# Performance work log

Measured on AMD Instinct MI355X. Metric: run time of the kernel, lower is better.

Reference implementation:

```python
import jax, jax.numpy as jnp
import numpy as np

N, F_IN, C, H, E, G = 10000, 128, 256, 4, 160000, 512
BN_EPS = 1e-5


def setup_inputs() -> dict:
    key = jax.random.key(0)
    ks = iter(jax.random.split(key, 40))
    nrm = lambda shape, s=0.05: jax.random.normal(next(ks), shape, jnp.float32) * s

    def bn(dim):
        # rows: gamma, beta, running_mean, running_var (eval-mode BatchNorm)
        g = 1.0 + jax.random.normal(next(ks), (dim,), jnp.float32) * 0.1
        b = jax.random.normal(next(ks), (dim,), jnp.float32) * 0.1
        m = jax.random.normal(next(ks), (dim,), jnp.float32) * 0.1
        v = jax.random.uniform(next(ks), (dim,), jnp.float32, 0.5, 1.5)
        return jnp.stack([g, b, m, v])  # [4, dim]

    x = jax.random.normal(next(ks), (N, F_IN), jnp.float32)
    edge_index = jax.random.randint(next(ks), (2, E), 0, N, jnp.int64)
    batch = (jnp.arange(N, dtype=jnp.int64) * G) // N  # sorted, every graph non-empty

    return {
        "x": x, "edge_index": edge_index, "batch": batch,
        "W1": nrm((F_IN, H * C)), "att_src1": nrm((H, C)), "att_dst1": nrm((H, C)), "b1": nrm((H * C,)), "bn1": bn(H * C),
        "W2": nrm((H * C, H * C)), "att_src2": nrm((H, C)), "att_dst2": nrm((H, C)), "b2": nrm((H * C,)), "bn2": bn(H * C),
        "W3": nrm((H * C, C)), "att_src3": nrm((1, C)), "att_dst3": nrm((1, C)), "b3": nrm((C,)), "bn3": bn(C),
        "fc1_w": nrm((3 * C, 2 * C)), "fc1_b": nrm((2 * C,)), "bnf1": bn(2 * C),
        "fc2_w": nrm((2 * C, C)), "fc2_b": nrm((C,)), "bnf2": bn(C),
        "fc3_w": nrm((C, 1)), "fc3_b": nrm((1,)),
    }


def batchnorm(x, p):
    g, b, m, v = p
    return (x - m) * (g * jax.lax.rsqrt(v + BN_EPS)) + b


def gat_conv(x, src, dst, W, att_src, att_dst, bias, heads):
    n = x.shape[0]
    h = (x @ W).reshape(n, heads, -1)                      # [N,H,C]
    a_src = jnp.einsum('nhc,hc->nh', h, att_src)           # [N,H]
    a_dst = jnp.einsum('nhc,hc->nh', h, att_dst)
    logits = jax.nn.leaky_relu(a_src[src] + a_dst[dst], 0.2)  # [E,H]
    # scatter-softmax over incoming edges of each destination node
    m = jax.ops.segment_max(logits, dst, num_segments=n)
    m = jax.lax.stop_gradient(jnp.where(jnp.isfinite(m), m, 0.0))
    e = jnp.exp(logits - m[dst])
    denom = jax.ops.segment_sum(e, dst, num_segments=n)
    alpha = e / (denom[dst] + 1e-16)                       # [E,H]
    msg = h[src] * alpha[:, :, None]                       # [E,H,C]
    out = jax.ops.segment_sum(msg, dst, num_segments=n)    # [N,H,C]
    return out.reshape(n, -1) + bias


def reference(x, edge_index, batch,
              W1, att_src1, att_dst1, b1, bn1,
              W2, att_src2, att_dst2, b2, bn2,
              W3, att_src3, att_dst3, b3, bn3,
              fc1_w, fc1_b, bnf1, fc2_w, fc2_b, bnf2, fc3_w, fc3_b):
    src, dst = edge_index[0], edge_index[1]
    h = jax.nn.elu(batchnorm(gat_conv(x, src, dst, W1, att_src1, att_dst1, b1, H), bn1))
    h = jax.nn.elu(batchnorm(gat_conv(h, src, dst, W2, att_src2, att_dst2, b2, H), bn2))
    h = jax.nn.elu(batchnorm(gat_conv(h, src, dst, W3, att_src3, att_dst3, b3, 1), bn3))
    # multi-pool readout over graphs
    s = jax.ops.segment_sum(h, batch, num_segments=G)
    cnt = jax.ops.segment_sum(jnp.ones((h.shape[0], 1), h.dtype), batch, num_segments=G)
    mean = s / cnt
    mx = jax.ops.segment_max(h, batch, num_segments=G)
    z = jnp.concatenate([mean, mx, s], axis=1)             # [G, 3C]
    z = jax.nn.relu(batchnorm(z @ fc1_w + fc1_b, bnf1))    # dropout: eval mode (identity)
    z = jax.nn.relu(batchnorm(z @ fc2_w + fc2_b, bnf2))
    return z @ fc3_w + fc3_b                               # [G, 1]
```

## Files before the change

### kernel.cpp

```cpp
#include <hip/hip_runtime.h>
#include <math.h>

#define N_NODES 10000
#define N_EDGES 160000
#define N_GRAPH 512

#define NEG_INF (-1e30f)

typedef __attribute__((ext_vector_type(8))) short s16x8;
typedef __attribute__((ext_vector_type(4))) float f32x4;

__device__ __forceinline__ unsigned short f2b(float f) {
  union { float f; unsigned u; } c{f};
  unsigned u = c.u;
  return (unsigned short)((u + 0x7fff + ((u >> 16) & 1)) >> 16);
}
__device__ __forceinline__ float b2f(unsigned short h) {
  union { unsigned u; float f; } c{(unsigned)h << 16};
  return c.f;
}

#define GLL16(gp, lp)                                                          \
  __builtin_amdgcn_global_load_lds(                                            \
      (const __attribute__((address_space(1))) unsigned int*)(gp),             \
      (__attribute__((address_space(3))) unsigned int*)(lp), 16, 0, 0)

__global__ void k_count(const int* __restrict__ dst, const int* __restrict__ batch,
                        int* __restrict__ deg, int* __restrict__ gcnt) {
  int i = blockIdx.x * 256 + threadIdx.x;
  if (i < N_EDGES) atomicAdd(&deg[dst[i]], 1);
  if (i < N_NODES) atomicAdd(&gcnt[batch[i]], 1);
}

__global__ void k_scan(const int* __restrict__ in, int* __restrict__ out, int n) {
  __shared__ int buf[1024];
  __shared__ int carry_s;
  if (threadIdx.x == 0) carry_s = 0;
  __syncthreads();
  for (int base = 0; base < n; base += 1024) {
    int i = base + (int)threadIdx.x;
    int v = (i < n) ? in[i] : 0;
    buf[threadIdx.x] = v;
    __syncthreads();
    for (int off = 1; off < 1024; off <<= 1) {
      int t = (threadIdx.x >= (unsigned)off) ? buf[threadIdx.x - off] : 0;
      __syncthreads();
      buf[threadIdx.x] += t;
      __syncthreads();
    }
    int carry = carry_s;
    if (i < n) out[i] = carry + buf[threadIdx.x] - v;
    __syncthreads();
    if (threadIdx.x == 0) carry_s = carry + buf[1023];
    __syncthreads();
  }
  if (threadIdx.x == 0) out[n] = carry_s;
}

__global__ void k_fill(const int* __restrict__ src, const int* __restrict__ dst,
                       const int* __restrict__ rowoff, int* __restrict__ cursor,
                       int* __restrict__ csr) {
  int e = blockIdx.x * 256 + threadIdx.x;
  if (e < N_EDGES) {
    int d = dst[e];
    int p = atomicAdd(&cursor[d], 1);
    csr[rowoff[d] + p] = src[e];
  }
}

__global__ __launch_bounds__(256) void k_sortseg(const int* __restrict__ rowoff,
                                                 int* __restrict__ vals) {
  const int node = blockIdx.x * 4 + (threadIdx.x >> 6);
  if (node >= N_NODES) return;
  const int lane = threadIdx.x & 63;
  const int a = rowoff[node], b = rowoff[node + 1];
  const int deg = b - a;
  if (deg <= 1) return;
  if (deg <= 64) {
    int v = (lane < deg) ? vals[a + lane] : 0x7fffffff;
#pragma unroll
    for (int ph = 0; ph < 64; ++ph) {
      const int par = ph & 1;
      const bool left = ((lane & 1) == par);
      const int partner = left ? lane + 1 : lane - 1;
      const int pv = __shfl(v, partner & 63);
      if (partner >= 0 && partner < 64) v = left ? min(v, pv) : max(v, pv);
    }
    if (lane < deg) vals[a + lane] = v;
  } else if (lane == 0) {
    for (int p = a + 1; p < b; ++p) {
      int v = vals[p];
      int q = p - 1;
      while (q >= a && vals[q] > v) { vals[q + 1] = vals[q]; --q; }
      vals[q + 1] = v;
    }
  }
}

__global__ void k_f2b4(const float* __restrict__ in, unsigned short* __restrict__ out, int n4) {
  int i = blockIdx.x * 256 + threadIdx.x;
  if (i < n4) {
    float4 v = ((const float4*)in)[i];
    ushort4 o;
    o.x = f2b(v.x); o.y = f2b(v.y); o.z = f2b(v.z); o.w = f2b(v.w);
    ((ushort4*)out)[i] = o;
  }
}

__global__ __launch_bounds__(256) void k_convT(const float* __restrict__ in,
                                               unsigned short* __restrict__ out,
                                               int K, int M) {
  __shared__ float t[32][33];
  const int mb = blockIdx.x * 32, kb = blockIdx.y * 32;
  const int tx = threadIdx.x & 31, ty = threadIdx.x >> 5;
#pragma unroll
  for (int r = ty; r < 32; r += 8) t[r][tx] = in[(size_t)(kb + r) * M + mb + tx];
  __syncthreads();
#pragma unroll
  for (int r = ty; r < 32; r += 8)
    out[(size_t)(mb + r) * K + kb + tx] = f2b(t[tx][r]);
}

__global__ __launch_bounds__(256) void k_gemm_bf16(
    const unsigned short* __restrict__ A, const unsigned short* __restrict__ Bt,
    unsigned short* __restrict__ Cbf, int M, int N, int K) {
  __shared__ unsigned short As[128 * 32];
  __shared__ unsigned short Bs[128 * 32];
  const int tid = threadIdx.x;
  const int lane = tid & 63, wave = tid >> 6;
  const int wr = wave >> 1, wc = wave & 1;
  const int m0 = blockIdx.y * 128, n0 = blockIdx.x * 128;

  f32x4 acc[4][4];
#pragma unroll
  for (int i = 0; i < 4; ++i)
#pragma unroll
    for (int j = 0; j < 4; ++j) acc[i][j] = (f32x4){0.f, 0.f, 0.f, 0.f};

  const int l4 = lane >> 2;
  const int kp8 = (lane & 3) * 8;
  int rA0 = m0 + wave * 32 + l4;
  int rA1 = rA0 + 16;
  rA0 = min(rA0, M - 1);
  rA1 = min(rA1, M - 1);
  const int rB0 = n0 + wave * 32 + l4;
  const int rB1 = rB0 + 16;
  const unsigned short* pA0 = A + (size_t)rA0 * K + kp8;
  const unsigned short* pA1 = A + (size_t)rA1 * K + kp8;
  const unsigned short* pB0 = Bt + (size_t)rB0 * K + kp8;
  const unsigned short* pB1 = Bt + (size_t)rB1 * K + kp8;
  unsigned short* lA = As + wave * 1024;
  unsigned short* lB = Bs + wave * 1024;

  const int fr = lane & 15, kg = (lane >> 4) * 8;

  for (int kb = 0; kb < K; kb += 32) {
    GLL16(pA0 + kb, lA);
    GLL16(pA1 + kb, lA + 512);
    GLL16(pB0 + kb, lB);
    GLL16(pB1 + kb, lB + 512);
    __syncthreads();

    s16x8 a[4], b[4];
#pragma unroll
    for (int m = 0; m < 4; ++m)
      a[m] = *(const s16x8*)&As[(wr * 64 + m * 16 + fr) * 32 + kg];
#pragma unroll
    for (int n = 0; n < 4; ++n)
      b[n] = *(const s16x8*)&Bs[(wc * 64 + n * 16 + fr) * 32 + kg];
#pragma unroll
    for (int m = 0; m < 4; ++m)
#pragma unroll
      for (int n = 0; n < 4; ++n)
        acc[m][n] = __builtin_amdgcn_mfma_f32_16x16x32_bf16(a[m], b[n], acc[m][n], 0, 0, 0);
    __syncthreads();
  }

  const int frow = (lane >> 4) * 4;
#pragma unroll
  for (int m = 0; m < 4; ++m) {
#pragma unroll
    for (int r = 0; r < 4; ++r) {
      const int row = m0 + wr * 64 + m * 16 + frow + r;
      if (row < M) {
#pragma unroll
        for (int n = 0; n < 4; ++n) {
          const int col = n0 + wc * 64 + n * 16 + fr;
          Cbf[(size_t)row * N + col] = f2b(acc[m][n][r]);
        }
      }
    }
  }
}

template <int K, int M>
__global__ __launch_bounds__(256) void k_head_fc(
    const float* __restrict__ A, const float* __restrict__ W,
    float* __restrict__ C, const float* __restrict__ bias,
    const float* __restrict__ bn) {
  constexpr int KQ = K / 4;
  __shared__ float Ap[8 * K];
  __shared__ float part[4][8][64];
  const int tid = threadIdx.x;
  const int g0 = blockIdx.y * 8;
  const int m0 = blockIdx.x * 64;
  const int c = tid & 63;
  const int q = tid >> 6;

  for (int i = tid; i < 8 * K / 4; i += 256)
    ((float4*)Ap)[i] = ((const float4*)(A + (size_t)g0 * K))[i];
  __syncthreads();

  float acc[8];
#pragma unroll
  for (int r = 0; r < 8; ++r) acc[r] = 0.f;

  const float* Wc = W + m0 + c;
  const int k0 = q * KQ;
  for (int k = k0; k < k0 + KQ; k += 4) {
    float wv[4];
#pragma unroll
    for (int u = 0; u < 4; ++u) wv[u] = Wc[(size_t)(k + u) * M];
#pragma unroll
    for (int r = 0; r < 8; ++r) {
      const float4 a4 = *(const float4*)&Ap[r * K + k];
      acc[r] += a4.x * wv[0] + a4.y * wv[1] + a4.z * wv[2] + a4.w * wv[3];
    }
  }

#pragma unroll
  for (int r = 0; r < 8; ++r) part[q][r][c] = acc[r];
  __syncthreads();

  for (int i = tid; i < 512; i += 256) {
    const int r = i >> 6, cc = i & 63;
    float v = part[0][r][cc] + part[1][r][cc] + part[2][r][cc] + part[3][r][cc];
    const int gc = m0 + cc;
    v += bias[gc];
    const float g = bn[gc], b = bn[M + gc], mu = bn[2 * M + gc], var = bn[3 * M + gc];
    v = (v - mu) * (g * rsqrtf(var + 1e-5f)) + b;
    v = fmaxf(v, 0.f);
    C[(size_t)(g0 + r) * M + gc] = v;
  }
}

template <int HEADS>
__global__ __launch_bounds__(64) void k_att(const unsigned short* __restrict__ h,
                                            const float* __restrict__ att_s,
                                            const float* __restrict__ att_d,
                                            float* __restrict__ aS,
                                            float* __restrict__ aD) {
  const int b = blockIdx.x;
  const int node = b / HEADS, hd = b % HEADS;
  const int lane = threadIdx.x;
  const unsigned short* row = h + (size_t)node * HEADS * 256 + hd * 256;
  const ushort4 v = *(const ushort4*)&row[lane * 4];
  const float4 s4 = *(const float4*)&att_s[hd * 256 + lane * 4];
  const float4 d4 = *(const float4*)&att_d[hd * 256 + lane * 4];
  float ss = b2f(v.x) * s4.x + b2f(v.y) * s4.y + b2f(v.z) * s4.z + b2f(v.w) * s4.w;
  float sd = b2f(v.x) * d4.x + b2f(v.y) * d4.y + b2f(v.z) * d4.z + b2f(v.w) * d4.w;
#pragma unroll
  for (int off = 32; off; off >>= 1) {
    ss += __shfl_xor(ss, off);
    sd += __shfl_xor(sd, off);
  }
  if (lane == 0) {
    aS[node * HEADS + hd] = ss;
    aD[node * HEADS + hd] = sd;
  }
}

template <int HEADS, int OUTBF>
__global__ __launch_bounds__(256) void k_gat_agg(
    const unsigned short* __restrict__ hpre, const float* __restrict__ aS,
    const float* __restrict__ aD, const int* __restrict__ rowoff,
    const int* __restrict__ csr, const float* __restrict__ bias,
    const float* __restrict__ bn, unsigned short* __restrict__ outb,
    float* __restrict__ outf) {
  constexpr int HC = HEADS * 256;
  constexpr int CPT = HC / 256;
  const int node = blockIdx.x;
  const int tid = threadIdx.x;
  const int lane = tid & 63, wave = tid >> 6;
  const int r0 = rowoff[node], r1 = rowoff[node + 1];
  const int deg = r1 - r0;

  __shared__ float s_m[HEADS], s_d[HEADS];
  __shared__ float s_alpha[HEADS * 64];
  __shared__ int s_src[64];

  if (wave < HEADS) {
    const float adn = aD[node * HEADS + wave];
    float mx = NEG_INF;
    for (int i = lane; i < deg; i += 64) {
      int s = csr[r0 + i];
      float l = aS[s * HEADS + wave] + adn;
      l = l > 0.f ? l : 0.2f * l;
      mx = fmaxf(mx, l);
    }
#pragma unroll
    for (int off = 32; off; off >>= 1) mx = fmaxf(mx, __shfl_xor(mx, off));
    float sum = 0.f;
    for (int i = lane; i < deg; i += 64) {
      int s = csr[r0 + i];
      float l = aS[s * HEADS + wave] + adn;
      l = l > 0.f ? l : 0.2f * l;
      sum += __expf(l - mx);
    }
#pragma unroll
    for (int off = 32; off; off >>= 1) sum += __shfl_xor(sum, off);
    if (lane == 0) {
      s_m[wave] = mx;
      s_d[wave] = 1.f / (sum + 1e-16f);
    }
  }
  __syncthreads();

  float acc[CPT];
#pragma unroll
  for (int j = 0; j < CPT; ++j) acc[j] = 0.f;
  const int c0 = tid * CPT;
  const int head = c0 / 256;

  for (int e0 = 0; e0 < deg; e0 += 64) {
    const int cnt = min(64, deg - e0);
    const int eL = tid & 63, hh = tid >> 6;
    if (hh < HEADS && eL < cnt) {
      int s = csr[r0 + e0 + eL];
      if (hh == 0) s_src[eL] = s;
      float l = aS[s * HEADS + hh] + aD[node * HEADS + hh];
      l = l > 0.f ? l : 0.2f * l;
      s_alpha[hh * 64 + eL] = __expf(l - s_m[hh]) * s_d[hh];
    }
    __syncthreads();
    for (int e = 0; e < cnt; ++e) {
      const int s = s_src[e];
      const float al = s_alpha[head * 64 + e];
      if constexpr (CPT == 4) {
        const ushort4 v = *(const ushort4*)(hpre + (size_t)s * HC + c0);
        acc[0] += al * b2f(v.x);
        acc[1] += al * b2f(v.y);
        acc[2] += al * b2f(v.z);
        acc[3] += al * b2f(v.w);
      } else {
        acc[0] += al * b2f(hpre[(size_t)s * HC + c0]);
      }
    }
    __syncthreads();
  }

  if constexpr (CPT == 4) {
    float rr[4];
#pragma unroll
    for (int j = 0; j < 4; ++j) {
      int c = c0 + j;
      float v = acc[j] + bias[c];
      float g = bn[c], b = bn[HC + c], mu = bn[2 * HC + c], var = bn[3 * HC + c];
      v = (v - mu) * (g * rsqrtf(var + 1e-5f)) + b;
      v = v > 0.f ? v : (__expf(v) - 1.f);
      rr[j] = v;
    }
    if (OUTBF) {
      ushort4 o;
      o.x = f2b(rr[0]); o.y = f2b(rr[1]); o.z = f2b(rr[2]); o.w = f2b(rr[3]);
      *(ushort4*)&outb[(size_t)node * HC + c0] = o;
    } else {
      *(float4*)&outf[(size_t)node * HC + c0] = *(const float4*)rr;
    }
  } else {
    int c = c0;
    float v = acc[0] + bias[c];
    float g = bn[c], b = bn[HC + c], mu = bn[2 * HC + c], var = bn[3 * HC + c];
    v = (v - mu) * (g * rsqrtf(var + 1e-5f)) + b;
    v = v > 0.f ? v : (__expf(v) - 1.f);
    if (OUTBF) outb[(size_t)node * HC + c] = f2b(v);
    else outf[(size_t)node * HC + c] = v;
  }
}

__global__ __launch_bounds__(256) void k_pool(const float* __restrict__ h,
                                              const int* __restrict__ goff,
                                              float* __restrict__ z) {
  const int g = blockIdx.x;
  const int c = threadIdx.x;
  const int i0 = goff[g], i1 = goff[g + 1];
  float s = 0.f, mx = NEG_INF;
  for (int i = i0; i < i1; ++i) {
    float v = h[(size_t)i * 256 + c];
    s += v;
    mx = fmaxf(mx, v);
  }
  const float cnt = (float)(i1 - i0);
  z[(size_t)g * 768 + c] = s / cnt;
  z[(size_t)g * 768 + 256 + c] = mx;
  z[(size_t)g * 768 + 512 + c] = s;
}

__global__ __launch_bounds__(64) void k_fc3(const float* __restrict__ z2,
                                            const float* __restrict__ w,
                                            const float* __restrict__ b,
                                            float* __restrict__ out) {
  const int g = blockIdx.x;
  const int lane = threadIdx.x;
  float s = 0.f;
#pragma unroll
  for (int j = 0; j < 4; ++j) {
    int c = lane + 64 * j;
    s += z2[(size_t)g * 256 + c] * w[c];
  }
#pragma unroll
  for (int off = 32; off; off >>= 1) s += __shfl_xor(s, off);
  if (lane == 0) out[g] = s + b[0];
}

extern "C" void kernel_launch(void* const* d_in, const int* in_sizes, int n_in,
                              void* d_out, int out_size, void* d_ws, size_t ws_size,
                              hipStream_t stream) {
  const float* x    = (const float*)d_in[0];
  const int* ei     = (const int*)d_in[1];
  const int* batch  = (const int*)d_in[2];
  const float* W1   = (const float*)d_in[3];
  const float* as1  = (const float*)d_in[4];
  const float* ad1  = (const float*)d_in[5];
  const float* b1   = (const float*)d_in[6];
  const float* bn1  = (const float*)d_in[7];
  const float* W2   = (const float*)d_in[8];
  const float* as2  = (const float*)d_in[9];
  const float* ad2  = (const float*)d_in[10];
  const float* b2   = (const float*)d_in[11];
  const float* bn2  = (const float*)d_in[12];
  const float* W3   = (const float*)d_in[13];
  const float* as3  = (const float*)d_in[14];
  const float* ad3  = (const float*)d_in[15];
  const float* b3   = (const float*)d_in[16];
  const float* bn3  = (const float*)d_in[17];
  const float* fc1w = (const float*)d_in[18];
  const float* fc1b = (const float*)d_in[19];
  const float* bnf1 = (const float*)d_in[20];
  const float* fc2w = (const float*)d_in[21];
  const float* fc2b = (const float*)d_in[22];
  const float* bnf2 = (const float*)d_in[23];
  const float* fc3w = (const float*)d_in[24];
  const float* fc3b = (const float*)d_in[25];
  float* out = (float*)d_out;

  const int* e_src = ei;
  const int* e_dst = ei + N_EDGES;

  char* w = (char*)d_ws;
  auto alloc = [&](size_t bytes) -> void* {
    void* p = (void*)w;
    w += (bytes + 255) & ~(size_t)255;
    return p;
  };
  unsigned short* x_bf  = (unsigned short*)alloc((size_t)N_NODES * 128 * 2);
  unsigned short* W1t   = (unsigned short*)alloc((size_t)1024 * 128 * 2);
  unsigned short* W2t   = (unsigned short*)alloc((size_t)1024 * 1024 * 2);
  unsigned short* W3t   = (unsigned short*)alloc((size_t)256 * 1024 * 2);
  unsigned short* hA_bf = (unsigned short*)alloc((size_t)N_NODES * 1024 * 2);
  unsigned short* hB_bf = (unsigned short*)alloc((size_t)N_NODES * 1024 * 2);
  float* hB_f32 = (float*)alloc((size_t)N_NODES * 256 * 4);
  float* aS   = (float*)alloc((size_t)N_NODES * 4 * 4);
  float* aD   = (float*)alloc((size_t)N_NODES * 4 * 4);
  int* deg    = (int*)alloc((size_t)(2 * N_NODES + N_GRAPH) * 4);
  int* cursor = deg + N_NODES;
  int* gcnt   = deg + 2 * N_NODES;
  int* rowoff = (int*)alloc((size_t)(N_NODES + 1) * 4);
  int* goff   = (int*)alloc((size_t)(N_GRAPH + 1) * 4);
  int* csr    = (int*)alloc((size_t)N_EDGES * 4);
  float* z    = (float*)alloc((size_t)N_GRAPH * 768 * 4);
  float* z1   = (float*)alloc((size_t)N_GRAPH * 512 * 4);
  float* z2   = (float*)alloc((size_t)N_GRAPH * 256 * 4);

  hipMemsetAsync(deg, 0, (size_t)(2 * N_NODES + N_GRAPH) * 4, stream);

  k_f2b4<<<(N_NODES * 128 / 4 + 255) / 256, 256, 0, stream>>>(x, x_bf, N_NODES * 128 / 4);
  k_convT<<<dim3(1024 / 32, 128 / 32), 256, 0, stream>>>(W1, W1t, 128, 1024);
  k_convT<<<dim3(1024 / 32, 1024 / 32), 256, 0, stream>>>(W2, W2t, 1024, 1024);
  k_convT<<<dim3(256 / 32, 1024 / 32), 256, 0, stream>>>(W3, W3t, 1024, 256);

  k_count<<<(N_EDGES + 255) / 256, 256, 0, stream>>>(e_dst, batch, deg, gcnt);
  k_scan<<<1, 1024, 0, stream>>>(deg, rowoff, N_NODES);
  k_scan<<<1, 1024, 0, stream>>>(gcnt, goff, N_GRAPH);
  k_fill<<<(N_EDGES + 255) / 256, 256, 0, stream>>>(e_src, e_dst, rowoff, cursor, csr);
  k_sortseg<<<(N_NODES + 3) / 4, 256, 0, stream>>>(rowoff, csr);

  const int mt = (N_NODES + 127) / 128;

  k_gemm_bf16<<<dim3(1024 / 128, mt), 256, 0, stream>>>(x_bf, W1t, hA_bf, N_NODES, 1024, 128);
  k_att<4><<<N_NODES * 4, 64, 0, stream>>>(hA_bf, as1, ad1, aS, aD);
  k_gat_agg<4, 1><<<N_NODES, 256, 0, stream>>>(hA_bf, aS, aD, rowoff, csr, b1, bn1, hB_bf, nullptr);

  k_gemm_bf16<<<dim3(1024 / 128, mt), 256, 0, stream>>>(hB_bf, W2t, hA_bf, N_NODES, 1024, 1024);
  k_att<4><<<N_NODES * 4, 64, 0, stream>>>(hA_bf, as2, ad2, aS, aD);
  k_gat_agg<4, 1><<<N_NODES, 256, 0, stream>>>(hA_bf, aS, aD, rowoff, csr, b2, bn2, hB_bf, nullptr);

  k_gemm_bf16<<<dim3(256 / 128, mt), 256, 0, stream>>>(hB_bf, W3t, hA_bf, N_NODES, 256, 1024);
  k_att<1><<<N_NODES, 64, 0, stream>>>(hA_bf, as3, ad3, aS, aD);
  k_gat_agg<1, 0><<<N_NODES, 256, 0, stream>>>(hA_bf, aS, aD, rowoff, csr, b3, bn3, nullptr, hB_f32);

  k_pool<<<N_GRAPH, 256, 0, stream>>>(hB_f32, goff, z);
  k_head_fc<768, 512><<<dim3(512 / 64, N_GRAPH / 8), 256, 0, stream>>>(z, fc1w, z1, fc1b, bnf1);
  k_head_fc<512, 256><<<dim3(256 / 64, N_GRAPH / 8), 256, 0, stream>>>(z1, fc2w, z2, fc2b, bnf2);
  k_fc3<<<N_GRAPH, 64, 0, stream>>>(z2, fc3w, fc3b, out);
}
```

Measured before the change: 342.7 us.

## Aggregate GAT edges with one wavefront per node and fused single-pass softmax

Replaces the block-per-node GAT aggregation kernel with two specialised kernels (4-head and 1-head) that assign one 64-lane wavefront per destination node, four nodes per block. For nodes with at most 64 incoming edges, the softmax max, sum and normalisation are computed in registers in one pass using wave shuffles. Block-wide barriers are removed, and each lane gathers source rows with 16-byte vector loads while unpacking bf16 pairs. The goal is to cut synchronisation overhead and idle threads on low-degree nodes. The cost is higher register use (16 accumulators per lane) and a multi-pass fallback for high-degree nodes.

```diff
diff --git a/kernel.cpp b/kernel.cpp
--- a/kernel.cpp
+++ b/kernel.cpp
@@ -19,6 +19,11 @@
   union { unsigned u; float f; } c{(unsigned)h << 16};
   return c.f;
 }
+__device__ __forceinline__ void up2(unsigned d, float& lo, float& hi) {
+  union { unsigned u; float f; } a{d << 16}, b{d & 0xffff0000u};
+  lo = a.f; hi = b.f;
+}
+__device__ __forceinline__ float lrelu(float x) { return x > 0.f ? x : 0.2f * x; }
 
 #define GLL16(gp, lp)                                                          \
   __builtin_amdgcn_global_load_lds(                                            \
@@ -270,112 +275,316 @@
   }
 }
 
-template <int HEADS, int OUTBF>
-__global__ __launch_bounds__(256) void k_gat_agg(
+__global__ __launch_bounds__(256) void k_aggw4(
     const unsigned short* __restrict__ hpre, const float* __restrict__ aS,
     const float* __restrict__ aD, const int* __restrict__ rowoff,
     const int* __restrict__ csr, const float* __restrict__ bias,
-    const float* __restrict__ bn, unsigned short* __restrict__ outb,
-    float* __restrict__ outf) {
-  constexpr int HC = HEADS * 256;
-  constexpr int CPT = HC / 256;
-  const int node = blockIdx.x;
-  const int tid = threadIdx.x;
-  const int lane = tid & 63, wave = tid >> 6;
-  const int r0 = rowoff[node], r1 = rowoff[node + 1];
-  const int deg = r1 - r0;
-
-  __shared__ float s_m[HEADS], s_d[HEADS];
-  __shared__ float s_alpha[HEADS * 64];
-  __shared__ int s_src[64];
-
-  if (wave < HEADS) {
-    const float adn = aD[node * HEADS + wave];
-    float mx = NEG_INF;
-    for (int i = lane; i < deg; i += 64) {
-      int s = csr[r0 + i];
-      float l = aS[s * HEADS + wave] + adn;
-      l = l > 0.f ? l : 0.2f * l;
-      mx = fmaxf(mx, l);
-    }
-#pragma unroll
-    for (int off = 32; off; off >>= 1) mx = fmaxf(mx, __shfl_xor(mx, off));
-    float sum = 0.f;
-    for (int i = lane; i < deg; i += 64) {
-      int s = csr[r0 + i];
-      float l = aS[s * HEADS + wave] + adn;
-      l = l > 0.f ? l : 0.2f * l;
-      sum += __expf(l - mx);
-    }
-#pragma unroll
-    for (int off = 32; off; off >>= 1) sum += __shfl_xor(sum, off);
-    if (lane == 0) {
-      s_m[wave] = mx;
-      s_d[wave] = 1.f / (sum + 1e-16f);
-    }
-  }
-  __syncthreads();
-
-  float acc[CPT];
-#pragma unroll
-  for (int j = 0; j < CPT; ++j) acc[j] = 0.f;
-  const int c0 = tid * CPT;
-  const int head = c0 / 256;
-
-  for (int e0 = 0; e0 < deg; e0 += 64) {
-    const int cnt = min(64, deg - e0);
-    const int eL = tid & 63, hh = tid >> 6;
-    if (hh < HEADS && eL < cnt) {
-      int s = csr[r0 + e0 + eL];
-      if (hh == 0) s_src[eL] = s;
-      float l = aS[s * HEADS + hh] + aD[node * HEADS + hh];
-      l = l > 0.f ? l : 0.2f * l;
-      s_alpha[hh * 64 + eL] = __expf(l - s_m[hh]) * s_d[hh];
-    }
-    __syncthreads();
-    for (int e = 0; e < cnt; ++e) {
+    const float* __restrict__ bn, unsigned short* __restrict__ outb) {
+  const int wv = threadIdx.x >> 6;
+  const int lane = threadIdx.x & 63;
+  const int node = blockIdx.x * 4 + wv;
+  if (node >= N_NODES) return;
+
+  __shared__ int s_src_all[4][64];
+  __shared__ float s_alp_all[4][64][4];
+  int* s_src = s_src_all[wv];
+  float (*s_alp)[4] = s_alp_all[wv];
+
+  const int r0 = rowoff[node];
+  const int deg = rowoff[node + 1] - r0;
+  const float4 ad4 = *(const float4*)&aD[(size_t)node * 4];
+
+  float acc[16];
+#pragma unroll
+  for (int j = 0; j < 16; ++j) acc[j] = 0.f;
+
+  const int g = lane >> 5;
+  const int g2 = g * 2;
+
+  auto gather = [&](int cnt) {
+    int e = 0;
+    for (; e + 2 <= cnt; e += 2) {
+      const int s0 = s_src[e], s1 = s_src[e + 1];
+      const float2 a0 = *(const float2*)&s_alp[e][g2];
+      const float2 a1 = *(const float2*)&s_alp[e + 1][g2];
+      const uint4* p0 = (const uint4*)(hpre + ((size_t)s0 << 10));
+      const uint4* p1 = (const uint4*)(hpre + ((size_t)s1 << 10));
+      const uint4 va0 = p0[lane], vb0 = p0[64 + lane];
+      const uint4 va1 = p1[lane], vb1 = p1[64 + lane];
+      float lo, hi;
+      up2(va0.x, lo, hi); acc[0] += a0.x * lo; acc[1] += a0.x * hi;
+      up2(va0.y, lo, hi); acc[2] += a0.x * lo; acc[3] += a0.x * hi;
+      up2(va0.z, lo, hi); acc[4] += a0.x * lo; acc[5] += a0.x * hi;
+      up2(va0.w, lo, hi); acc[6] += a0.x * lo; acc[7] += a0.x * hi;
+      up2(vb0.x, lo, hi); acc[8] += a0.y * lo; acc[9] += a0.y * hi;
+      up2(vb0.y, lo, hi); acc[10] += a0.y * lo; acc[11] += a0.y * hi;
+      up2(vb0.z, lo, hi); acc[12] += a0.y * lo; acc[13] += a0.y * hi;
+      up2(vb0.w, lo, hi); acc[14] += a0.y * lo; acc[15] += a0.y * hi;
+      up2(va1.x, lo, hi); acc[0] += a1.x * lo; acc[1] += a1.x * hi;
+      up2(va1.y, lo, hi); acc[2] += a1.x * lo; acc[3] += a1.x * hi;
+      up2(va1.z, lo, hi); acc[4] += a1.x * lo; acc[5] += a1.x * hi;
+      up2(va1.w, lo, hi); acc[6] += a1.x * lo; acc[7] += a1.x * hi;
+      up2(vb1.x, lo, hi); acc[8] += a1.y * lo; acc[9] += a1.y * hi;
+      up2(vb1.y, lo, hi); acc[10] += a1.y * lo; acc[11] += a1.y * hi;
+      up2(vb1.z, lo, hi); acc[12] += a1.y * lo; acc[13] += a1.y * hi;
+      up2(vb1.w, lo, hi); acc[14] += a1.y * lo; acc[15] += a1.y * hi;
+    }
+    if (e < cnt) {
+      const int s0 = s_src[e];
+      const float2 a0 = *(const float2*)&s_alp[e][g2];
+      const uint4* p0 = (const uint4*)(hpre + ((size_t)s0 << 10));
+      const uint4 va0 = p0[lane], vb0 = p0[64 + lane];
+      float lo, hi;
+      up2(va0.x, lo, hi); acc[0] += a0.x * lo; acc[1] += a0.x * hi;
+      up2(va0.y, lo, hi); acc[2] += a0.x * lo; acc[3] += a0.x * hi;
+      up2(va0.z, lo, hi); acc[4] += a0.x * lo; acc[5] += a0.x * hi;
+      up2(va0.w, lo, hi); acc[6] += a0.x * lo; acc[7] += a0.x * hi;
+      up2(vb0.x, lo, hi); acc[8] += a0.y * lo; acc[9] += a0.y * hi;
+      up2(vb0.y, lo, hi); acc[10] += a0.y * lo; acc[11] += a0.y * hi;
+      up2(vb0.z, lo, hi); acc[12] += a0.y * lo; acc[13] += a0.y * hi;
+      up2(vb0.w, lo, hi); acc[14] += a0.y * lo; acc[15] += a0.y * hi;
+    }
+  };
+
+  if (deg <= 64) {
+    float l0, l1, l2, l3;
+    int sE = 0;
+    const bool act = lane < deg;
+    if (act) {
+      sE = csr[r0 + lane];
+      const float4 sv = *(const float4*)&aS[(size_t)sE * 4];
+      l0 = lrelu(sv.x + ad4.x);
+      l1 = lrelu(sv.y + ad4.y);
+      l2 = lrelu(sv.z + ad4.z);
+      l3 = lrelu(sv.w + ad4.w);
+    } else {
+      l0 = l1 = l2 = l3 = NEG_INF;
+    }
+    float m0 = l0, m1 = l1, m2 = l2, m3 = l3;
+#pragma unroll
+    for (int off = 32; off; off >>= 1) {
+      m0 = fmaxf(m0, __shfl_xor(m0, off));
+      m1 = fmaxf(m1, __shfl_xor(m1, off));
+      m2 = fmaxf(m2, __shfl_xor(m2, off));
+      m3 = fmaxf(m3, __shfl_xor(m3, off));
+    }
+    float e0 = act ? __expf(l0 - m0) : 0.f;
+    float e1 = act ? __expf(l1 - m1) : 0.f;
+    float e2 = act ? __expf(l2 - m2) : 0.f;
+    float e3 = act ? __expf(l3 - m3) : 0.f;
+    float s0 = e0, s1 = e1, s2 = e2, s3 = e3;
+#pragma unroll
+    for (int off = 32; off; off >>= 1) {
+      s0 += __shfl_xor(s0, off);
+      s1 += __shfl_xor(s1, off);
+      s2 += __shfl_xor(s2, off);
+      s3 += __shfl_xor(s3, off);
+    }
+    if (act) {
+      s_src[lane] = sE;
+      s_alp[lane][0] = e0 / (s0 + 1e-16f);
+      s_alp[lane][1] = e2 / (s2 + 1e-16f);
+      s_alp[lane][2] = e1 / (s1 + 1e-16f);
+      s_alp[lane][3] = e3 / (s3 + 1e-16f);
+    }
+    gather(deg);
+  } else {
+    auto logits = [&](int idx, float& a, float& b, float& c, float& d, int& s) {
+      s = csr[r0 + idx];
+      const float4 sv = *(const float4*)&aS[(size_t)s * 4];
+      a = lrelu(sv.x + ad4.x);
+      b = lrelu(sv.y + ad4.y);
+      c = lrelu(sv.z + ad4.z);
+      d = lrelu(sv.w + ad4.w);
+    };
+    float m0 = NEG_INF, m1 = NEG_INF, m2 = NEG_INF, m3 = NEG_INF;
+    for (int base = 0; base < deg; base += 64) {
+      if (base + lane < deg) {
+        float a, b, c, d; int s;
+        logits(base + lane, a, b, c, d, s);
+        m0 = fmaxf(m0, a); m1 = fmaxf(m1, b); m2 = fmaxf(m2, c); m3 = fmaxf(m3, d);
+      }
+    }
+#pragma unroll
+    for (int off = 32; off; off >>= 1) {
+      m0 = fmaxf(m0, __shfl_xor(m0, off));
+      m1 = fmaxf(m1, __shfl_xor(m1, off));
+      m2 = fmaxf(m2, __shfl_xor(m2, off));
+      m3 = fmaxf(m3, __shfl_xor(m3, off));
+    }
+    float s0 = 0.f, s1 = 0.f, s2 = 0.f, s3 = 0.f;
+    for (int base = 0; base < deg; base += 64) {
+      if (base + lane < deg) {
+        float a, b, c, d; int s;
+        logits(base + lane, a, b, c, d, s);
+        s0 += __expf(a - m0); s1 += __expf(b - m1);
+        s2 += __expf(c - m2); s3 += __expf(d - m3);
+      }
+    }
+#pragma unroll
+    for (int off = 32; off; off >>= 1) {
+      s0 += __shfl_xor(s0, off);
+      s1 += __shfl_xor(s1, off);
+      s2 += __shfl_xor(s2, off);
+      s3 += __shfl_xor(s3, off);
+    }
+    const float d0 = 1.f / (s0 + 1e-16f), d1 = 1.f / (s1 + 1e-16f);
+    const float d2 = 1.f / (s2 + 1e-16f), d3 = 1.f / (s3 + 1e-16f);
+    for (int base = 0; base < deg; base += 64) {
+      const int cnt = min(64, deg - base);
+      if (lane < cnt) {
+        float a, b, c, d; int s;
+        logits(base + lane, a, b, c, d, s);
+        s_src[lane] = s;
+        s_alp[lane][0] = __expf(a - m0) * d0;
+        s_alp[lane][1] = __expf(c - m2) * d2;
+        s_alp[lane][2] = __expf(b - m1) * d1;
+        s_alp[lane][3] = __expf(d - m3) * d3;
+      }
+      gather(cnt);
+    }
+  }
+
+#pragma unroll
+  for (int half = 0; half < 2; ++half) {
+    const int cb = half * 512 + lane * 8;
+    const float* ap = acc + half * 8;
+    unsigned od[4];
+#pragma unroll
+    for (int jj = 0; jj < 2; ++jj) {
+      const float4 bi = *(const float4*)&bias[cb + jj * 4];
+      const float4 gg = *(const float4*)&bn[cb + jj * 4];
+      const float4 bb = *(const float4*)&bn[1024 + cb + jj * 4];
+      const float4 mm = *(const float4*)&bn[2048 + cb + jj * 4];
+      const float4 vv = *(const float4*)&bn[3072 + cb + jj * 4];
+      float r[4];
+#pragma unroll
+      for (int j = 0; j < 4; ++j) {
+        float v = ap[jj * 4 + j] + ((const float*)&bi)[j];
+        v = (v - ((const float*)&mm)[j]) *
+                (((const float*)&gg)[j] * rsqrtf(((const float*)&vv)[j] + 1e-5f)) +
+            ((const float*)&bb)[j];
+        v = v > 0.f ? v : (__expf(v) - 1.f);
+        r[j] = v;
+      }
+      od[jj * 2 + 0] = (unsigned)f2b(r[0]) | ((unsigned)f2b(r[1]) << 16);
+      od[jj * 2 + 1] = (unsigned)f2b(r[2]) | ((unsigned)f2b(r[3]) << 16);
+    }
+    *(uint4*)&outb[((size_t)node << 10) + cb] = make_uint4(od[0], od[1], od[2], od[3]);
+  }
+}
+
+__global__ __launch_bounds__(256) void k_aggw1(
+    const unsigned short* __restrict__ hpre, const float* __restrict__ aS,
+    const float* __restrict__ aD, const int* __restrict__ rowoff,
+    const int* __restrict__ csr, const float* __restrict__ bias,
+    const float* __restrict__ bn, float* __restrict__ outf) {
+  const int wv = threadIdx.x >> 6;
+  const int lane = threadIdx.x & 63;
+  const int node = blockIdx.x * 4 + wv;
+  if (node >= N_NODES) return;
+
+  __shared__ int s_src_all[4][64];
+  __shared__ float s_alp_all[4][64];
+  int* s_src = s_src_all[wv];
+  float* s_alp = s_alp_all[wv];
+
+  const int r0 = rowoff[node];
+  const int deg = rowoff[node + 1] - r0;
+  const float ad = aD[node];
+
+  float acc[4] = {0.f, 0.f, 0.f, 0.f};
+
+  auto gather = [&](int cnt) {
+    int e = 0;
+    for (; e + 4 <= cnt; e += 4) {
+      uint2 v[4];
+      float al[4];
+#pragma unroll
+      for (int u = 0; u < 4; ++u) {
+        const int s = s_src[e + u];
+        al[u] = s_alp[e + u];
+        v[u] = ((const uint2*)(hpre + ((size_t)s << 8)))[lane];
+      }
+#pragma unroll
+      for (int u = 0; u < 4; ++u) {
+        float lo, hi;
+        up2(v[u].x, lo, hi); acc[0] += al[u] * lo; acc[1] += al[u] * hi;
+        up2(v[u].y, lo, hi); acc[2] += al[u] * lo; acc[3] += al[u] * hi;
+      }
+    }
+    for (; e < cnt; ++e) {
       const int s = s_src[e];
-      const float al = s_alpha[head * 64 + e];
-      if constexpr (CPT == 4) {
-        const ushort4 v = *(const ushort4*)(hpre + (size_t)s * HC + c0);
-        acc[0] += al * b2f(v.x);
-        acc[1] += al * b2f(v.y);
-        acc[2] += al * b2f(v.z);
-        acc[3] += al * b2f(v.w);
-      } else {
-        acc[0] += al * b2f(hpre[(size_t)s * HC + c0]);
+      const float al = s_alp[e];
+      const uint2 v = ((const uint2*)(hpre + ((size_t)s << 8)))[lane];
+      float lo, hi;
+      up2(v.x, lo, hi); acc[0] += al * lo; acc[1] += al * hi;
+      up2(v.y, lo, hi); acc[2] += al * lo; acc[3] += al * hi;
+    }
+  };
+
+  if (deg <= 64) {
+    float l0;
+    int sE = 0;
+    const bool act = lane < deg;
+    if (act) {
+      sE = csr[r0 + lane];
+      l0 = lrelu(aS[sE] + ad);
+    } else {
+      l0 = NEG_INF;
+    }
+    float m0 = l0;
+#pragma unroll
+    for (int off = 32; off; off >>= 1) m0 = fmaxf(m0, __shfl_xor(m0, off));
+    float e0 = act ? __expf(l0 - m0) : 0.f;
+    float s0 = e0;
+#pragma unroll
+    for (int off = 32; off; off >>= 1) s0 += __shfl_xor(s0, off);
+    if (act) {
+      s_src[lane] = sE;
+      s_alp[lane] = e0 / (s0 + 1e-16f);
+    }
+    gather(deg);
+  } else {
+    float m0 = NEG_INF;
+    for (int base = 0; base < deg; base += 64)
+      if (base + lane < deg) m0 = fmaxf(m0, lrelu(aS[csr[r0 + base + lane]] + ad));
+#pragma unroll
+    for (int off = 32; off; off >>= 1) m0 = fmaxf(m0, __shfl_xor(m0, off));
+    float s0 = 0.f;
+    for (int base = 0; base < deg; base += 64)
+      if (base + lane < deg) s0 += __expf(lrelu(aS[csr[r0 + base + lane]] + ad) - m0);
+#pragma unroll
+    for (int off = 32; off; off >>= 1) s0 += __shfl_xor(s0, off);
+    const float d0 = 1.f / (s0 + 1e-16f);
+    for (int base = 0; base < deg; base += 64) {
+      const int cnt = min(64, deg - base);
+      if (lane < cnt) {
+        const int s = csr[r0 + base + lane];
+        s_src[lane] = s;
+        s_alp[lane] = __expf(lrelu(aS[s] + ad) - m0) * d0;
       }
-    }
-    __syncthreads();
-  }
-
-  if constexpr (CPT == 4) {
-    float rr[4];
-#pragma unroll
-    for (int j = 0; j < 4; ++j) {
-      int c = c0 + j;
-      float v = acc[j] + bias[c];
-      float g = bn[c], b = bn[HC + c], mu = bn[2 * HC + c], var = bn[3 * HC + c];
-      v = (v - mu) * (g * rsqrtf(var + 1e-5f)) + b;
-      v = v > 0.f ? v : (__expf(v) - 1.f);
-      rr[j] = v;
-    }
-    if (OUTBF) {
-      ushort4 o;
-      o.x = f2b(rr[0]); o.y = f2b(rr[1]); o.z = f2b(rr[2]); o.w = f2b(rr[3]);
-      *(ushort4*)&outb[(size_t)node * HC + c0] = o;
-    } else {
-      *(float4*)&outf[(size_t)node * HC + c0] = *(const float4*)rr;
-    }
-  } else {
-    int c = c0;
-    float v = acc[0] + bias[c];
-    float g = bn[c], b = bn[HC + c], mu = bn[2 * HC + c], var = bn[3 * HC + c];
-    v = (v - mu) * (g * rsqrtf(var + 1e-5f)) + b;
+      gather(cnt);
+    }
+  }
+
+  const int c = lane * 4;
+  const float4 bi = *(const float4*)&bias[c];
+  const float4 gg = *(const float4*)&bn[c];
+  const float4 bb = *(const float4*)&bn[256 + c];
+  const float4 mm = *(const float4*)&bn[512 + c];
+  const float4 vv = *(const float4*)&bn[768 + c];
+  float4 o;
+#pragma unroll
+  for (int j = 0; j < 4; ++j) {
+    float v = acc[j] + ((const float*)&bi)[j];
+    v = (v - ((const float*)&mm)[j]) *
+            (((const float*)&gg)[j] * rsqrtf(((const float*)&vv)[j] + 1e-5f)) +
+        ((const float*)&bb)[j];
     v = v > 0.f ? v : (__expf(v) - 1.f);
-    if (OUTBF) outb[(size_t)node * HC + c] = f2b(v);
-    else outf[(size_t)node * HC + c] = v;
-  }
+    ((float*)&o)[j] = v;
+  }
+  *(float4*)&outf[((size_t)node << 8) + c] = o;
 }
 
 __global__ __launch_bounds__(256) void k_pool(const float* __restrict__ h,
@@ -486,18 +695,19 @@
   k_sortseg<<<(N_NODES + 3) / 4, 256, 0, stream>>>(rowoff, csr);
 
   const int mt = (N_NODES + 127) / 128;
+  const int nb = (N_NODES + 3) / 4;
 
   k_gemm_bf16<<<dim3(1024 / 128, mt), 256, 0, stream>>>(x_bf, W1t, hA_bf, N_NODES, 1024, 128);
   k_att<4><<<N_NODES * 4, 64, 0, stream>>>(hA_bf, as1, ad1, aS, aD);
-  k_gat_agg<4, 1><<<N_NODES, 256, 0, stream>>>(hA_bf, aS, aD, rowoff, csr, b1, bn1, hB_bf, nullptr);
+  k_aggw4<<<nb, 256, 0, stream>>>(hA_bf, aS, aD, rowoff, csr, b1, bn1, hB_bf);
 
   k_gemm_bf16<<<dim3(1024 / 128, mt), 256, 0, stream>>>(hB_bf, W2t, hA_bf, N_NODES, 1024, 1024);
   k_att<4><<<N_NODES * 4, 64, 0, stream>>>(hA_bf, as2, ad2, aS, aD);
-  k_gat_agg<4, 1><<<N_NODES, 256, 0, stream>>>(hA_bf, aS, aD, rowoff, csr, b2, bn2, hB_bf, nullptr);
+  k_aggw4<<<nb, 256, 0, stream>>>(hA_bf, aS, aD, rowoff, csr, b2, bn2, hB_bf);
 
   k_gemm_bf16<<<dim3(256 / 128, mt), 256, 0, stream>>>(hB_bf, W3t, hA_bf, N_NODES, 256, 1024);
   k_att<1><<<N_NODES, 64, 0, stream>>>(hA_bf, as3, ad3, aS, aD);
-  k_gat_agg<1, 0><<<N_NODES, 256, 0, stream>>>(hA_bf, aS, aD, rowoff, csr, b3, bn3, nullptr, hB_f32);
+  k_aggw1<<<nb, 256, 0, stream>>>(hA_bf, aS, aD, rowoff, csr, b3, bn3, hB_f32);
 
   k_pool<<<N_GRAPH, 256, 0, stream>>>(hB_f32, goff, z);
   k_head_fc<768, 512><<<dim3(512 / 64, N_GRAPH / 8), 256, 0, stream>>>(z, fc1w, z1, fc1b, bnf1);
```

After: 321.2 us. 1.07x faster.
